# Performance work log

Hardware: AMD Instinct MI355X
Metric: run time of the kernel (lower is better)

Reference implementation:

```python
import jax, jax.numpy as jnp
import numpy as np

EPS = 1e-5

def _rmsnorm(x):
    # BitLinear applies a (non-learnable) RMSNorm to activations before quantization
    return x * jax.lax.rsqrt(jnp.mean(x * x, axis=-1, keepdims=True) + EPS)

def _activation_quant(x):
    # per-token absmax int8 quantization, dequantized back to float
    scale = 127.0 / jnp.clip(jnp.max(jnp.abs(x), axis=-1, keepdims=True), EPS, None)
    return jnp.clip(jnp.round(x * scale), -128, 127) / scale

def _weight_quant(w):
    # absmean ternary {-1,0,1} quantization, dequantized back to float
    scale = 1.0 / jnp.clip(jnp.mean(jnp.abs(w)), EPS, None)
    return jnp.clip(jnp.round(w * scale), -1, 1) / scale

def _bitlinear(x, w):
    xn = _rmsnorm(x)
    # straight-through estimators (identity grads through quantizers)
    xq = xn + jax.lax.stop_gradient(_activation_quant(xn) - xn)
    wq = w + jax.lax.stop_gradient(_weight_quant(w) - w)
    return jnp.einsum('bsd,hd->bsh', xq, wq)

def setup_inputs() -> dict:
    key = jax.random.key(0)
    k1, k2, k3, k4 = jax.random.split(key, 4)
    B, S, D, H = 4, 2048, 4096, 11008
    return {
        'x': jax.random.normal(k1, (B, S, D), dtype=jnp.float32),
        'w_gate': jax.random.normal(k2, (H, D), dtype=jnp.float32) * 0.02,
        'w_up': jax.random.normal(k3, (H, D), dtype=jnp.float32) * 0.02,
        'w_down': jax.random.normal(k4, (D, H), dtype=jnp.float32) * 0.02,
    }

def reference(x, w_gate, w_up, w_down):
    h = jax.nn.silu(_bitlinear(x, w_gate)) * _bitlinear(x, w_up)
    return _bitlinear(h, w_down)
```

## Files before the change

kernel.cpp:

```cpp
#include <hip/hip_runtime.h>
#include <hip/hip_bf16.h>
#include <cstdint>

#define EPS 1e-5

typedef __attribute__((ext_vector_type(4))) int int32x4;

__device__ __forceinline__ void gload(const char* g, char* l) {
  __builtin_amdgcn_global_load_lds(
      (const __attribute__((address_space(1))) unsigned int*)g,
      (__attribute__((address_space(3))) unsigned int*)l, 16, 0, 0);
}

__device__ inline float np_leaf_abs(const float* __restrict__ a, int n) {
  float r[8];
  #pragma unroll
  for (int j = 0; j < 8; j++) r[j] = fabsf(a[j]);
  for (int i = 8; i < n; i += 8) {
    #pragma unroll
    for (int j = 0; j < 8; j++) r[j] += fabsf(a[i + j]);
  }
  return ((r[0] + r[1]) + (r[2] + r[3])) + ((r[4] + r[5]) + (r[6] + r[7]));
}

__global__ __launch_bounds__(256) void np_blocksums(
    const float* __restrict__ w, float* __restrict__ bs) {
  int b = blockIdx.x * 256 + threadIdx.x;
  const float* a = w + (long)b * 344;
  float s0 = np_leaf_abs(a, 80);
  float s1 = np_leaf_abs(a + 80, 88);
  float s2 = np_leaf_abs(a + 168, 88);
  float s3 = np_leaf_abs(a + 256, 88);
  bs[b] = (s0 + s1) + (s2 + s3);
}

__global__ __launch_bounds__(256) void np_tree_partial(
    const float* __restrict__ bs, float* __restrict__ part) {
  __shared__ float sh[256];
  int t = threadIdx.x;
  const float* a = bs + (long)blockIdx.x * 512;
  sh[t] = a[2 * t] + a[2 * t + 1];
  __syncthreads();
  for (int n = 128; n >= 1; n >>= 1) {
    float x = 0.f;
    if (t < n) x = sh[2 * t] + sh[2 * t + 1];
    __syncthreads();
    if (t < n) sh[t] = x;
    __syncthreads();
  }
  if (t == 0) part[blockIdx.x] = sh[0];
}

__global__ __launch_bounds__(128) void np_tree_final(
    const float* __restrict__ part, float* __restrict__ out) {
  __shared__ float sh[128];
  int t = threadIdx.x;
  sh[t] = part[2 * t] + part[2 * t + 1];
  __syncthreads();
  for (int n = 64; n >= 1; n >>= 1) {
    float x = 0.f;
    if (t < n) x = sh[2 * t] + sh[2 * t + 1];
    __syncthreads();
    if (t < n) sh[t] = x;
    __syncthreads();
  }
  if (t == 0) out[0] = sh[0] / 45088768.0f;
}

__global__ __launch_bounds__(256) void quant_w(
    const float* __restrict__ w, const float* __restrict__ mean_ptr,
    char* __restrict__ q, long n4) {
  float scale = 1.0f / fmaxf(*mean_ptr, 1e-5f);
  long i = (long)blockIdx.x * blockDim.x + threadIdx.x;
  long stride = (long)gridDim.x * blockDim.x;
  const float4* w4 = (const float4*)w;
  char4* q4 = (char4*)q;
  for (; i < n4; i += stride) {
    float4 v = w4[i];
    char4 c;
    c.x = (char)(int)fminf(1.f, fmaxf(-1.f, rintf(v.x * scale)));
    c.y = (char)(int)fminf(1.f, fmaxf(-1.f, rintf(v.y * scale)));
    c.z = (char)(int)fminf(1.f, fmaxf(-1.f, rintf(v.z * scale)));
    c.w = (char)(int)fminf(1.f, fmaxf(-1.f, rintf(v.w * scale)));
    q4[i] = c;
  }
}

#define CORR_MAX 1024
#define WIN 1e-6f

__global__ __launch_bounds__(256) void quant_w_down(
    const float* __restrict__ w, const float* __restrict__ mean_ptr,
    char* __restrict__ q, int* __restrict__ cnt,
    int* __restrict__ ck, float* __restrict__ cv) {
  float scale = 1.0f / fmaxf(*mean_ptr, 1e-5f);
  long i0 = ((long)blockIdx.x * blockDim.x + threadIdx.x) * 4;
  long stride = (long)gridDim.x * blockDim.x * 4;
  for (long i = i0; i < 4096L * 11008L; i += stride) {
    char4 c;
    #pragma unroll
    for (int j = 0; j < 4; j++) {
      float t = w[i + j] * scale;
      float qv = fminf(1.f, fmaxf(-1.f, rintf(t)));
      if (fabsf(fabsf(t) - 0.5f) < WIN) {
        qv = 0.f;
        int idx = atomicAdd(cnt, 1);
        if (idx < CORR_MAX) {
          ck[idx] = (int)(i + j);
          cv[idx] = t > 0.f ? 0.5f : -0.5f;
        }
      }
      ((char*)&c)[j] = (char)(int)qv;
    }
    *(char4*)(q + i) = c;
  }
}

__global__ void zero_cnt(int* cnt) { *cnt = 0; }

__global__ __launch_bounds__(64) void apply_corr(
    const int* __restrict__ cnt, const int* __restrict__ ck,
    const float* __restrict__ cv, const char* __restrict__ qh,
    const float* __restrict__ fh, const float* __restrict__ meanw,
    float* __restrict__ out) {
  int r = blockIdx.x * 64 + threadIdx.x;
  float fwd = fmaxf(meanw[2], 1e-5f);
  int n = *cnt; if (n > CORR_MAX) n = CORR_MAX;
  float fr = fh[r] * fwd;
  for (int i = 0; i < n; i++) {
    int flat = ck[i];
    int nn = flat / 11008, kk = flat % 11008;
    float qv = (float)qh[(long)r * 11008 + kk];
    out[(long)r * 4096 + nn] += cv[i] * qv * fr;
  }
}

__device__ inline void block_reduce_sum_max_d(double& s, float& m) {
  #pragma unroll
  for (int off = 1; off < 64; off <<= 1) {
    s += __shfl_xor(s, off, 64);
    m = fmaxf(m, __shfl_xor(m, off, 64));
  }
  __shared__ double ssh[4];
  __shared__ float msh[4];
  int wv = threadIdx.x >> 6;
  if ((threadIdx.x & 63) == 0) { ssh[wv] = s; msh[wv] = m; }
  __syncthreads();
  s = (ssh[0] + ssh[1]) + (ssh[2] + ssh[3]);
  m = fmaxf(fmaxf(msh[0], msh[1]), fmaxf(msh[2], msh[3]));
}

__device__ inline char quant1d(float x, double rn, double s) {
  double t = (double)x * rn;
  double q = rint(t * s);
  q = fmin(127.0, fmax(-128.0, q));
  return (char)(int)q;
}

__global__ __launch_bounds__(256) void act_quant_x(
    const float* __restrict__ x, char* __restrict__ qx, float* __restrict__ fx) {
  const int row = blockIdx.x;
  const float4* xr = (const float4*)(x + (long)row * 4096);
  float4 v[4];
  double ss = 0.0;
  float am = 0.f;
  #pragma unroll
  for (int i = 0; i < 4; i++) {
    v[i] = xr[i * 256 + threadIdx.x];
    ss += ((double)v[i].x * v[i].x + (double)v[i].y * v[i].y) +
          ((double)v[i].z * v[i].z + (double)v[i].w * v[i].w);
    am = fmaxf(am, fmaxf(fmaxf(fabsf(v[i].x), fabsf(v[i].y)),
                         fmaxf(fabsf(v[i].z), fabsf(v[i].w))));
  }
  block_reduce_sum_max_d(ss, am);
  double rn = 1.0 / sqrt(ss / 4096.0 + EPS);
  double den = fmax((double)am * rn, EPS);
  double s = 127.0 / den;
  if (threadIdx.x == 0) fx[row] = (float)(den / 127.0);
  char4* qr = (char4*)(qx + (long)row * 4096);
  #pragma unroll
  for (int i = 0; i < 4; i++) {
    char4 c;
    c.x = quant1d(v[i].x, rn, s);
    c.y = quant1d(v[i].y, rn, s);
    c.z = quant1d(v[i].z, rn, s);
    c.w = quant1d(v[i].w, rn, s);
    qr[i * 256 + threadIdx.x] = c;
  }
}

__global__ __launch_bounds__(256) void act_quant_h(
    const float* __restrict__ h, char* __restrict__ qh, float* __restrict__ fh) {
  const long row = blockIdx.x;
  const float4* hr = (const float4*)(h + row * 11008);
  double ss = 0.0;
  float am = 0.f;
  for (int i = threadIdx.x; i < 2752; i += 256) {
    float4 v = hr[i];
    ss += ((double)v.x * v.x + (double)v.y * v.y) +
          ((double)v.z * v.z + (double)v.w * v.w);
    am = fmaxf(am, fmaxf(fmaxf(fabsf(v.x), fabsf(v.y)),
                         fmaxf(fabsf(v.z), fabsf(v.w))));
  }
  block_reduce_sum_max_d(ss, am);
  double rn = 1.0 / sqrt(ss / 11008.0 + EPS);
  double den = fmax((double)am * rn, EPS);
  double s = 127.0 / den;
  if (threadIdx.x == 0) fh[row] = (float)(den / 127.0);
  char4* qr = (char4*)(qh + row * 11008);
  for (int i = threadIdx.x; i < 2752; i += 256) {
    float4 v = hr[i];
    char4 c;
    c.x = quant1d(v.x, rn, s);
    c.y = quant1d(v.y, rn, s);
    c.z = quant1d(v.z, rn, s);
    c.w = quant1d(v.w, rn, s);
    qr[i] = c;
  }
}


__global__ __launch_bounds__(256, 2) void gemm_gateup(
    const char* __restrict__ qx, const char* __restrict__ qwg, const char* __restrict__ qwu,
    const float* __restrict__ meanw, const float* __restrict__ fx, float* __restrict__ h) {
  __shared__ __align__(16) char As[2][8192];
  __shared__ __align__(16) char Bgs[2][8192];
  __shared__ __align__(16) char Bus[2][8192];
  const int t = threadIdx.x;
  const int lane = t & 63;
  const int wv = t >> 6;
  const int m0 = blockIdx.x * 128;
  const int n0 = blockIdx.y * 128;
  const int wm = (wv >> 1) * 64;
  const int wn = (wv & 1) * 64;

  const int rowin = lane >> 2;
  const int gcol = (((lane & 3) - ((lane >> 3) & 3)) & 3) * 16;
  const int loff = (lane & 15) * 64 + ((((lane >> 4) + ((lane >> 1) & 3)) & 3) << 4);

  const char* gA0 = qx  + (long)(m0 + 32 * wv + rowin) * 4096 + gcol;
  const char* gG0 = qwg + (long)(n0 + 32 * wv + rowin) * 4096 + gcol;
  const char* gU0 = qwu + (long)(n0 + 32 * wv + rowin) * 4096 + gcol;
  const long R16 = 16L * 4096;

  int32x4 accg[4][4] = {};
  int32x4 accu[4][4] = {};

  #define STAGE_GU(pb, k0)                                   \
    do {                                                     \
      gload(gA0 + (k0),       &As [pb][wv * 2048]);          \
      gload(gA0 + (k0) + R16, &As [pb][wv * 2048 + 1024]);   \
      gload(gG0 + (k0),       &Bgs[pb][wv * 2048]);          \
      gload(gG0 + (k0) + R16, &Bgs[pb][wv * 2048 + 1024]);   \
      gload(gU0 + (k0),       &Bus[pb][wv * 2048]);          \
      gload(gU0 + (k0) + R16, &Bus[pb][wv * 2048 + 1024]);   \
    } while (0)

  STAGE_GU(0, 0);
  __syncthreads();
  for (int ks = 0; ks < 64; ++ks) {
    int pb = ks & 1;
    if (ks + 1 < 64) STAGE_GU(pb ^ 1, (ks + 1) * 64);
    const char* ab = &As [pb][0] + wm * 64 + loff;
    const char* gb = &Bgs[pb][0] + wn * 64 + loff;
    const char* ub = &Bus[pb][0] + wn * 64 + loff;
    int32x4 a[4];
    #pragma unroll
    for (int m = 0; m < 4; m++) a[m] = *(const int32x4*)(ab + m * 1024);
    #pragma unroll
    for (int n = 0; n < 4; n++) {
      int32x4 bg = *(const int32x4*)(gb + n * 1024);
      int32x4 bu = *(const int32x4*)(ub + n * 1024);
      #pragma unroll
      for (int m = 0; m < 4; m++) {
        accg[m][n] = __builtin_amdgcn_mfma_i32_16x16x64_i8(a[m], bg, accg[m][n], 0, 0, 0);
        accu[m][n] = __builtin_amdgcn_mfma_i32_16x16x64_i8(a[m], bu, accu[m][n], 0, 0, 0);
      }
    }
    if (ks + 1 < 64) __syncthreads();
  }
  #undef STAGE_GU

  float fwg = fmaxf(meanw[0], 1e-5f);
  float fwu = fmaxf(meanw[1], 1e-5f);
  const int rgrp = lane >> 4;
  const int cidx = lane & 15;
  #pragma unroll
  for (int m = 0; m < 4; m++) {
    #pragma unroll
    for (int r = 0; r < 4; r++) {
      int grow = m0 + wm + m * 16 + rgrp * 4 + r;
      float fxr = fx[grow];
      float sg = fxr * fwg, su = fxr * fwu;
      #pragma unroll
      for (int n = 0; n < 4; n++) {
        float g = (float)accg[m][n][r] * sg;
        float u = (float)accu[m][n][r] * su;
        float hv = g / (1.f + expf(-g)) * u;
        h[(long)grow * 11008 + (n0 + wn + n * 16 + cidx)] = hv;
      }
    }
  }
}

__global__ __launch_bounds__(256, 2) void gemm_down(
    const char* __restrict__ qh, const char* __restrict__ qwd,
    const float* __restrict__ mean_wd, const float* __restrict__ fh,
    float* __restrict__ out) {
  __shared__ __align__(16) char As[2][8192];
  __shared__ __align__(16) char Bs[2][8192];
  const int t = threadIdx.x;
  const int lane = t & 63;
  const int wv = t >> 6;
  const int m0 = blockIdx.x * 128;
  const int n0 = blockIdx.y * 128;
  const int wm = (wv >> 1) * 64;
  const int wn = (wv & 1) * 64;

  const int rowin = lane >> 2;
  const int gcol = (((lane & 3) - ((lane >> 3) & 3)) & 3) * 16;
  const int loff = (lane & 15) * 64 + ((((lane >> 4) + ((lane >> 1) & 3)) & 3) << 4);

  const char* gA0 = qh  + (long)(m0 + 32 * wv + rowin) * 11008 + gcol;
  const char* gB0 = qwd + (long)(n0 + 32 * wv + rowin) * 11008 + gcol;
  const long R16 = 16L * 11008;

  int32x4 acc[4][4] = {};

  #define STAGE_DN(pb, k0)                                  \
    do {                                                    \
      gload(gA0 + (k0),       &As[pb][wv * 2048]);          \
      gload(gA0 + (k0) + R16, &As[pb][wv * 2048 + 1024]);   \
      gload(gB0 + (k0),       &Bs[pb][wv * 2048]);          \
      gload(gB0 + (k0) + R16, &Bs[pb][wv * 2048 + 1024]);   \
    } while (0)

  STAGE_DN(0, 0);
  __syncthreads();
  for (int ks = 0; ks < 172; ++ks) {
    int pb = ks & 1;
    if (ks + 1 < 172) STAGE_DN(pb ^ 1, (ks + 1) * 64);
    const char* ab = &As[pb][0] + wm * 64 + loff;
    const char* bb = &Bs[pb][0] + wn * 64 + loff;
    int32x4 a[4];
    #pragma unroll
    for (int m = 0; m < 4; m++) a[m] = *(const int32x4*)(ab + m * 1024);
    #pragma unroll
    for (int n = 0; n < 4; n++) {
      int32x4 b = *(const int32x4*)(bb + n * 1024);
      #pragma unroll
      for (int m = 0; m < 4; m++)
        acc[m][n] = __builtin_amdgcn_mfma_i32_16x16x64_i8(a[m], b, acc[m][n], 0, 0, 0);
    }
    if (ks + 1 < 172) __syncthreads();
  }
  #undef STAGE_DN

  float fwd = fmaxf(mean_wd[0], 1e-5f);
  const int rgrp = lane >> 4;
  const int cidx = lane & 15;
  #pragma unroll
  for (int m = 0; m < 4; m++) {
    #pragma unroll
    for (int r = 0; r < 4; r++) {
      int grow = m0 + wm + m * 16 + rgrp * 4 + r;
      float f = fh[grow] * fwd;
      #pragma unroll
      for (int n = 0; n < 4; n++) {
        out[(long)grow * 4096 + (n0 + wn + n * 16 + cidx)] =
            (float)acc[m][n][r] * f;
      }
    }
  }
}

extern "C" void kernel_launch(void* const* d_in, const int* in_sizes, int n_in,
                              void* d_out, int out_size, void* d_ws, size_t ws_size,
                              hipStream_t stream) {
  const float* x      = (const float*)d_in[0];
  const float* w_gate = (const float*)d_in[1];
  const float* w_up   = (const float*)d_in[2];
  const float* w_down = (const float*)d_in[3];
  float* out = (float*)d_out;

  const long NW = 11008L * 4096L;
  const long NX = 8192L * 4096L;
  const long NH = 8192L * 11008L;

  char* ws  = (char*)d_ws;
  char* qwg = ws;
  char* qwu = qwg + NW;
  char* qwd = qwu + NW;
  char* qx  = qwd + NW;
  char* qh  = qx + NX;
  float* h  = (float*)(qh + NH);
  float* fx = h + NH;
  float* fh = fx + 8192;
  float* meanw = fh + 8192;
  float* bs    = meanw + 4;
  float* tmp   = bs + 131072;
  int*   ccnt  = (int*)(tmp + 65536);
  int*   ck    = ccnt + 4;
  float* cv    = (float*)(ck + CORR_MAX);

  zero_cnt<<<1, 1, 0, stream>>>(ccnt);

  np_blocksums<<<512, 256, 0, stream>>>(w_gate, bs);
  np_tree_partial<<<256, 256, 0, stream>>>(bs, tmp);
  np_tree_final<<<1, 128, 0, stream>>>(tmp, meanw + 0);
  np_blocksums<<<512, 256, 0, stream>>>(w_up, bs);
  np_tree_partial<<<256, 256, 0, stream>>>(bs, tmp);
  np_tree_final<<<1, 128, 0, stream>>>(tmp, meanw + 1);
  np_blocksums<<<512, 256, 0, stream>>>(w_down, bs);
  np_tree_partial<<<256, 256, 0, stream>>>(bs, tmp);
  np_tree_final<<<1, 128, 0, stream>>>(tmp, meanw + 2);

  quant_w<<<4096, 256, 0, stream>>>(w_gate, meanw + 0, qwg, NW / 4);
  quant_w<<<4096, 256, 0, stream>>>(w_up,   meanw + 1, qwu, NW / 4);
  quant_w_down<<<4096, 256, 0, stream>>>(w_down, meanw + 2, qwd, ccnt, ck, cv);

  act_quant_x<<<8192, 256, 0, stream>>>(x, qx, fx);

  gemm_gateup<<<dim3(64, 86), 256, 0, stream>>>(qx, qwg, qwu, meanw, fx, h);

  act_quant_h<<<8192, 256, 0, stream>>>(h, qh, fh);

  gemm_down<<<dim3(64, 32), 256, 0, stream>>>(qh, qwd, meanw + 2, fh, out);

  apply_corr<<<128, 64, 0, stream>>>(ccnt, ck, cv, qh, fh, meanw, out);
}
```

Measured before the change: 2.101 ms.

## Enlarge GEMM tiles to 8 waves, add triple-buffered LDS pipeline and block swizzle

Both int8 MFMA GEMMs move from 256-thread blocks with 128x128 tiles to 512-thread blocks with larger tiles: 128x256 for gate/up and 256x256 for down. Global-to-LDS staging becomes a three-stage ring driven by explicit s_waitcnt vmcnt plus s_barrier, replacing double buffering with a full __syncthreads per step. A 1D grid with a modular swizzle spreads adjacent block IDs across tiles so reuse in L2 improves. The cost is more LDS and registers per block (the down kernel holds 8x4 accumulators), which risks lower occupancy or spills, and the hand-counted vmcnt values must match the number of loads issued per stage.

```diff
diff --git a/kernel.cpp b/kernel.cpp
--- a/kernel.cpp
+++ b/kernel.cpp
@@ -220,50 +220,54 @@
 }
 
 
-__global__ __launch_bounds__(256, 2) void gemm_gateup(
+__global__ __launch_bounds__(512, 2) void gemm_gateup(
     const char* __restrict__ qx, const char* __restrict__ qwg, const char* __restrict__ qwu,
     const float* __restrict__ meanw, const float* __restrict__ fx, float* __restrict__ h) {
-  __shared__ __align__(16) char As[2][8192];
-  __shared__ __align__(16) char Bgs[2][8192];
-  __shared__ __align__(16) char Bus[2][8192];
+  __shared__ __align__(16) char As[3][8192];
+  __shared__ __align__(16) char Bgs[3][16384];
+  __shared__ __align__(16) char Bus[3][16384];
   const int t = threadIdx.x;
   const int lane = t & 63;
   const int wv = t >> 6;
-  const int m0 = blockIdx.x * 128;
-  const int n0 = blockIdx.y * 128;
-  const int wm = (wv >> 1) * 64;
-  const int wn = (wv & 1) * 64;
+  const int bid = blockIdx.x;
+  const int swz = (bid & 7) * 344 + (bid >> 3);
+  const int m0 = (swz & 63) * 128;
+  const int n0 = (swz >> 6) * 256;
+  const int wm = (wv >> 2) * 64;
+  const int wn = (wv & 3) * 64;
 
   const int rowin = lane >> 2;
   const int gcol = (((lane & 3) - ((lane >> 3) & 3)) & 3) * 16;
-  const int loff = (lane & 15) * 64 + ((((lane >> 4) + ((lane >> 1) & 3)) & 3) << 4);
-
-  const char* gA0 = qx  + (long)(m0 + 32 * wv + rowin) * 4096 + gcol;
-  const char* gG0 = qwg + (long)(n0 + 32 * wv + rowin) * 4096 + gcol;
-  const char* gU0 = qwu + (long)(n0 + 32 * wv + rowin) * 4096 + gcol;
+  const int slot = ((((lane >> 4) + ((lane >> 1) & 3)) & 3) << 4);
+  const int lrow = (lane & 15) * 64;
+
+  const char* gA = qx  + (long)(m0 + wv * 16 + rowin) * 4096 + gcol;
+  const char* gG = qwg + (long)(n0 + wv * 32 + rowin) * 4096 + gcol;
+  const char* gU = qwu + (long)(n0 + wv * 32 + rowin) * 4096 + gcol;
   const long R16 = 16L * 4096;
 
   int32x4 accg[4][4] = {};
   int32x4 accu[4][4] = {};
 
-  #define STAGE_GU(pb, k0)                                   \
-    do {                                                     \
-      gload(gA0 + (k0),       &As [pb][wv * 2048]);          \
-      gload(gA0 + (k0) + R16, &As [pb][wv * 2048 + 1024]);   \
-      gload(gG0 + (k0),       &Bgs[pb][wv * 2048]);          \
-      gload(gG0 + (k0) + R16, &Bgs[pb][wv * 2048 + 1024]);   \
-      gload(gU0 + (k0),       &Bus[pb][wv * 2048]);          \
-      gload(gU0 + (k0) + R16, &Bus[pb][wv * 2048 + 1024]);   \
+  #define STAGE_GU(pb, k0)                                 \
+    do {                                                   \
+      gload(gA + (k0),       &As [pb][wv * 1024]);         \
+      gload(gG + (k0),       &Bgs[pb][wv * 2048]);         \
+      gload(gG + (k0) + R16, &Bgs[pb][wv * 2048 + 1024]);  \
+      gload(gU + (k0),       &Bus[pb][wv * 2048]);         \
+      gload(gU + (k0) + R16, &Bus[pb][wv * 2048 + 1024]);  \
     } while (0)
 
   STAGE_GU(0, 0);
-  __syncthreads();
+  STAGE_GU(1, 64);
   for (int ks = 0; ks < 64; ++ks) {
-    int pb = ks & 1;
-    if (ks + 1 < 64) STAGE_GU(pb ^ 1, (ks + 1) * 64);
-    const char* ab = &As [pb][0] + wm * 64 + loff;
-    const char* gb = &Bgs[pb][0] + wn * 64 + loff;
-    const char* ub = &Bus[pb][0] + wn * 64 + loff;
+    const int pb = ks % 3;
+    if (ks < 63) asm volatile("s_waitcnt vmcnt(5)\n\ts_barrier" ::: "memory");
+    else         asm volatile("s_waitcnt vmcnt(0)\n\ts_barrier" ::: "memory");
+    if (ks + 2 < 64) STAGE_GU((ks + 2) % 3, (ks + 2) * 64);
+    const char* ab = &As [pb][0] + wm * 64 + lrow + slot;
+    const char* gb = &Bgs[pb][0] + wn * 64 + lrow + slot;
+    const char* ub = &Bus[pb][0] + wn * 64 + lrow + slot;
     int32x4 a[4];
     #pragma unroll
     for (int m = 0; m < 4; m++) a[m] = *(const int32x4*)(ab + m * 1024);
@@ -277,7 +281,6 @@
         accu[m][n] = __builtin_amdgcn_mfma_i32_16x16x64_i8(a[m], bu, accu[m][n], 0, 0, 0);
       }
     }
-    if (ks + 1 < 64) __syncthreads();
   }
   #undef STAGE_GU
 
@@ -303,56 +306,60 @@
   }
 }
 
-__global__ __launch_bounds__(256, 2) void gemm_down(
+__global__ __launch_bounds__(512, 2) void gemm_down(
     const char* __restrict__ qh, const char* __restrict__ qwd,
     const float* __restrict__ mean_wd, const float* __restrict__ fh,
     float* __restrict__ out) {
-  __shared__ __align__(16) char As[2][8192];
-  __shared__ __align__(16) char Bs[2][8192];
+  __shared__ __align__(16) char As[3][16384];
+  __shared__ __align__(16) char Bs[3][16384];
   const int t = threadIdx.x;
   const int lane = t & 63;
   const int wv = t >> 6;
-  const int m0 = blockIdx.x * 128;
-  const int n0 = blockIdx.y * 128;
-  const int wm = (wv >> 1) * 64;
-  const int wn = (wv & 1) * 64;
+  const int bid = blockIdx.x;
+  const int swz = (bid & 7) * 64 + (bid >> 3);
+  const int m0 = (swz & 31) * 256;
+  const int n0 = (swz >> 5) * 256;
+  const int wm = (wv >> 2) * 128;
+  const int wn = (wv & 3) * 64;
 
   const int rowin = lane >> 2;
   const int gcol = (((lane & 3) - ((lane >> 3) & 3)) & 3) * 16;
-  const int loff = (lane & 15) * 64 + ((((lane >> 4) + ((lane >> 1) & 3)) & 3) << 4);
-
-  const char* gA0 = qh  + (long)(m0 + 32 * wv + rowin) * 11008 + gcol;
-  const char* gB0 = qwd + (long)(n0 + 32 * wv + rowin) * 11008 + gcol;
+  const int slot = ((((lane >> 4) + ((lane >> 1) & 3)) & 3) << 4);
+  const int lrow = (lane & 15) * 64;
+
+  const char* gA = qh  + (long)(m0 + wv * 32 + rowin) * 11008 + gcol;
+  const char* gB = qwd + (long)(n0 + wv * 32 + rowin) * 11008 + gcol;
   const long R16 = 16L * 11008;
 
-  int32x4 acc[4][4] = {};
-
-  #define STAGE_DN(pb, k0)                                  \
-    do {                                                    \
-      gload(gA0 + (k0),       &As[pb][wv * 2048]);          \
-      gload(gA0 + (k0) + R16, &As[pb][wv * 2048 + 1024]);   \
-      gload(gB0 + (k0),       &Bs[pb][wv * 2048]);          \
-      gload(gB0 + (k0) + R16, &Bs[pb][wv * 2048 + 1024]);   \
+  int32x4 acc[8][4] = {};
+
+  #define STAGE_DN(pb, k0)                                \
+    do {                                                  \
+      gload(gA + (k0),       &As[pb][wv * 2048]);         \
+      gload(gA + (k0) + R16, &As[pb][wv * 2048 + 1024]);  \
+      gload(gB + (k0),       &Bs[pb][wv * 2048]);         \
+      gload(gB + (k0) + R16, &Bs[pb][wv * 2048 + 1024]);  \
     } while (0)
 
   STAGE_DN(0, 0);
-  __syncthreads();
+  STAGE_DN(1, 64);
   for (int ks = 0; ks < 172; ++ks) {
-    int pb = ks & 1;
-    if (ks + 1 < 172) STAGE_DN(pb ^ 1, (ks + 1) * 64);
-    const char* ab = &As[pb][0] + wm * 64 + loff;
-    const char* bb = &Bs[pb][0] + wn * 64 + loff;
-    int32x4 a[4];
-    #pragma unroll
-    for (int m = 0; m < 4; m++) a[m] = *(const int32x4*)(ab + m * 1024);
+    const int pb = ks % 3;
+    if (ks < 171) asm volatile("s_waitcnt vmcnt(4)\n\ts_barrier" ::: "memory");
+    else          asm volatile("s_waitcnt vmcnt(0)\n\ts_barrier" ::: "memory");
+    if (ks + 2 < 172) STAGE_DN((ks + 2) % 3, (ks + 2) * 64);
+    const char* ab = &As[pb][0] + wm * 64 + lrow + slot;
+    const char* bb = &Bs[pb][0] + wn * 64 + lrow + slot;
+    int32x4 a[8];
+    #pragma unroll
+    for (int m = 0; m < 8; m++) a[m] = *(const int32x4*)(ab + m * 1024);
     #pragma unroll
     for (int n = 0; n < 4; n++) {
       int32x4 b = *(const int32x4*)(bb + n * 1024);
       #pragma unroll
-      for (int m = 0; m < 4; m++)
+      for (int m = 0; m < 8; m++)
         acc[m][n] = __builtin_amdgcn_mfma_i32_16x16x64_i8(a[m], b, acc[m][n], 0, 0, 0);
     }
-    if (ks + 1 < 172) __syncthreads();
   }
   #undef STAGE_DN
 
@@ -360,7 +367,7 @@
   const int rgrp = lane >> 4;
   const int cidx = lane & 15;
   #pragma unroll
-  for (int m = 0; m < 4; m++) {
+  for (int m = 0; m < 8; m++) {
     #pragma unroll
     for (int r = 0; r < 4; r++) {
       int grow = m0 + wm + m * 16 + rgrp * 4 + r;
@@ -421,11 +428,11 @@
 
   act_quant_x<<<8192, 256, 0, stream>>>(x, qx, fx);
 
-  gemm_gateup<<<dim3(64, 86), 256, 0, stream>>>(qx, qwg, qwu, meanw, fx, h);
+  gemm_gateup<<<2752, 512, 0, stream>>>(qx, qwg, qwu, meanw, fx, h);
 
   act_quant_h<<<8192, 256, 0, stream>>>(h, qh, fh);
 
-  gemm_down<<<dim3(64, 32), 256, 0, stream>>>(qh, qwd, meanw + 2, fh, out);
+  gemm_down<<<512, 512, 0, stream>>>(qh, qwd, meanw + 2, fh, out);
 
   apply_corr<<<128, 64, 0, stream>>>(ccnt, ck, cv, qh, fh, meanw, out);
 }
```

Result: slower. 2.275 ms, median of 3 (+8.3%).
